# Optimization experiments

Measured on AMD Instinct MI355X. Metric: run time of the kernel, lower is better.

The kernel has to match this reference:

```python
import jax, jax.numpy as jnp
import numpy as np

N = 100000      # nodes
E = 1600000     # edges
IN_DIM = 256
HID = 64
NCLS = 32


def setup_inputs() -> dict:
    key = jax.random.key(0)
    ks = jax.random.split(key, 7)
    features = jax.random.normal(ks[0], (N, IN_DIM), dtype=jnp.float32)
    hidden_prev = jax.random.normal(ks[1], (N, HID), dtype=jnp.float32)
    adj_indices = jax.random.randint(ks[2], (2, E), 0, N, dtype=jnp.int32)
    # torch.rand init, scaled by 0.1 to keep activations numerically sane
    W0 = jax.random.uniform(ks[3], (IN_DIM, HID), dtype=jnp.float32) * 0.1
    W1 = jax.random.uniform(ks[4], (HID, HID), dtype=jnp.float32) * 0.1
    W2 = jax.random.uniform(ks[5], (HID, NCLS), dtype=jnp.float32) * 0.1
    att_w = jax.random.uniform(ks[6], (2 * HID, 1), dtype=jnp.float32) * 0.1
    return {"features": features, "hidden_prev": hidden_prev,
            "adj_indices": adj_indices, "W0": W0, "W1": W1, "W2": W2,
            "att_w": att_w}


def _edge_softmax(scores, rows, n):
    # sparse softmax over dim=1 of an NxN COO: normalize per source row
    m = jax.ops.segment_max(scores, rows, num_segments=n)
    ex = jnp.exp(scores - m[rows])
    s = jax.ops.segment_sum(ex, rows, num_segments=n)
    return ex / s[rows]


def _compute_attention(hfeat, adj_indices, att_w):
    src, dst = adj_indices[0], adj_indices[1]
    h = hfeat.shape[1]
    # cat(f_src, f_dst) @ att_w == f_src @ w_a + f_dst @ w_b ; project per-node
    proj_a = hfeat @ att_w[:h, 0]   # [N]
    proj_b = hfeat @ att_w[h:, 0]   # [N]
    scores = jax.nn.leaky_relu(proj_a[src] + proj_b[dst])  # [E]
    return _edge_softmax(scores, src, hfeat.shape[0])


def _spmm(att_vals, adj_indices, x):
    # out[i] = sum_{(i,j) in E} att * x[j]
    src, dst = adj_indices[0], adj_indices[1]
    return jax.ops.segment_sum(att_vals[:, None] * x[dst], src,
                               num_segments=x.shape[0])


def reference(features, hidden_prev, adj_indices, W0, W1, W2, att_w):
    att = _compute_attention(hidden_prev, adj_indices, att_w)  # [E]
    h = features
    for W in (W0, W1, W2):
        h = jax.nn.elu(_spmm(att, adj_indices, h @ W))
    return jax.nn.log_softmax(h, axis=1)
```

## Files before the change

### kernel.cpp

```cpp
#include <hip/hip_runtime.h>
#include <math.h>

#define HIDN 64
#define NCLS_K 32
#define INDIM 256
#define BSHIFT 7
#define MAXBUCK 1024
#define BUCK_CAP 4096
#define DSTBITS 17
#define DSTMASK ((1 << DSTBITS) - 1)
#define SCB 512

typedef unsigned int uint;
typedef unsigned short ushort;
typedef __attribute__((ext_vector_type(8))) short short8v;
typedef __attribute__((ext_vector_type(4))) float f32x4;

__device__ inline ushort f2bf(float f) {
  uint u = __float_as_uint(f);
  return (ushort)((u + 0x7FFFu + ((u >> 16) & 1u)) >> 16);
}
__device__ inline float bf2f(ushort h) { return __uint_as_float(((uint)h) << 16); }

__global__ __launch_bounds__(256) void proj_kernel(const float* __restrict__ hid,
    const float* __restrict__ attw, float* __restrict__ pa, float* __restrict__ pb, int n) {
  int wid  = (blockIdx.x * blockDim.x + threadIdx.x) >> 6;
  int lane = threadIdx.x & 63;
  if (wid >= n) return;
  float v = hid[(size_t)wid * HIDN + lane];
  float a = v * attw[lane];
  float b = v * attw[HIDN + lane];
  #pragma unroll
  for (int off = 32; off >= 1; off >>= 1) {
    a += __shfl_xor(a, off, 64);
    b += __shfl_xor(b, off, 64);
  }
  if (lane == 0) { pa[wid] = a; pb[wid] = b; }
}

__global__ __launch_bounds__(256) void hist2(const int* __restrict__ src,
    int* __restrict__ hmatT, int e, int nb, int nper) {
  __shared__ int h[MAXBUCK];
  int lo = blockIdx.x * nper;
  int hi = min(e, lo + nper);
  for (int j = threadIdx.x; j < nb; j += 256) h[j] = 0;
  __syncthreads();
  for (int i = lo + threadIdx.x; i < hi; i += 256)
    atomicAdd(&h[src[i] >> BSHIFT], 1);
  __syncthreads();
  for (int j = threadIdx.x; j < nb; j += 256)
    hmatT[(size_t)j * SCB + blockIdx.x] = h[j];
}

__global__ __launch_bounds__(256) void col_scan(int* __restrict__ hmatT,
    int* __restrict__ bcnt, int nb) {
  constexpr int PER = SCB / 64;
  int wv = blockIdx.x * 4 + (threadIdx.x >> 6);
  if (wv >= nb) return;
  int lane = threadIdx.x & 63;
  int* col = hmatT + (size_t)wv * SCB + lane * PER;
  int v[PER];
  int s = 0;
  #pragma unroll
  for (int q = 0; q < PER; ++q) { v[q] = col[q]; s += v[q]; }
  int x = s;
  #pragma unroll
  for (int off = 1; off < 64; off <<= 1) {
    int t = __shfl_up(x, off, 64);
    if (lane >= off) x += t;
  }
  int pre = x - s;
  #pragma unroll
  for (int q = 0; q < PER; ++q) { int t = v[q]; col[q] = pre; pre += t; }
  if (lane == 63) bcnt[wv] = pre;
}

__global__ __launch_bounds__(1024) void scan_buckets(const int* __restrict__ bcnt,
    int* __restrict__ bbase, int* __restrict__ rowp, int nb, int n, int e) {
  __shared__ int sm[1024];
  int tid = threadIdx.x;
  int v = (tid < nb) ? bcnt[tid] : 0;
  sm[tid] = v;
  __syncthreads();
  for (int off = 1; off < 1024; off <<= 1) {
    int t = (tid >= off) ? sm[tid - off] : 0;
    __syncthreads();
    sm[tid] += t;
    __syncthreads();
  }
  if (tid < nb) bbase[tid] = sm[tid] - v;
  if (tid == 0) { bbase[nb] = e; rowp[n] = e; }
}

__global__ __launch_bounds__(256) void scatter2(const int* __restrict__ src,
    const int* __restrict__ dst, const int* __restrict__ hmatT,
    const int* __restrict__ bbase, int* __restrict__ pairs, int e, int nb, int nper) {
  __shared__ int h[MAXBUCK];
  int lo = blockIdx.x * nper;
  int hi = min(e, lo + nper);
  for (int j = threadIdx.x; j < nb; j += 256)
    h[j] = bbase[j] + hmatT[(size_t)j * SCB + blockIdx.x];
  __syncthreads();
  for (int i = lo + threadIdx.x; i < hi; i += 256) {
    int s = src[i];
    int pos = atomicAdd(&h[s >> BSHIFT], 1);
    pairs[pos] = ((s & 127) << DSTBITS) | dst[i];
  }
}

__global__ __launch_bounds__(256) void build_csr(const int* __restrict__ pairs,
    const int* __restrict__ bbase, int* __restrict__ rowp,
    int* __restrict__ dstc, int n) {
  __shared__ int hist[128];
  __shared__ int cur[128];
  __shared__ int ord[BUCK_CAP];
  int b = blockIdx.x;
  int tid = threadIdx.x;
  int base = bbase[b];
  int m = bbase[b + 1] - base;
  if (tid < 128) hist[tid] = 0;
  __syncthreads();
  for (int i = tid; i < m; i += 256)
    atomicAdd(&hist[pairs[base + i] >> DSTBITS], 1);
  __syncthreads();
  int own = (tid < 128) ? hist[tid] : 0;
  for (int off = 1; off < 128; off <<= 1) {
    int t = (tid < 128 && tid >= off) ? hist[tid - off] : 0;
    __syncthreads();
    if (tid < 128) hist[tid] += t;
    __syncthreads();
  }
  if (tid < 128) {
    int excl = hist[tid] - own;
    cur[tid] = excl;
    int s = (b << BSHIFT) + tid;
    if (s < n) rowp[s] = base + excl;
  }
  __syncthreads();
  for (int i = tid; i < m; i += 256) {
    int key = pairs[base + i];
    int pos = atomicAdd(&cur[key >> DSTBITS], 1);
    ord[pos] = key;
  }
  __syncthreads();
  for (int i = tid; i < m; i += 256) dstc[base + i] = ord[i];
}

__device__ inline int wave_sort64(int key, int lane) {
  #pragma unroll
  for (int k = 2; k <= 64; k <<= 1) {
    #pragma unroll
    for (int j = k >> 1; j > 0; j >>= 1) {
      int p = __shfl_xor(key, j, 64);
      bool up    = ((lane & k) == 0);
      bool lower = ((lane & j) == 0);
      int mn = min(key, p), mx = max(key, p);
      key = (lower == up) ? mn : mx;
    }
  }
  return key;
}

__global__ __launch_bounds__(256) void att_softmax(const float* __restrict__ pa,
    const float* __restrict__ pb, int* __restrict__ dstc,
    const int* __restrict__ rowp, ushort* __restrict__ attb, int n) {
  int wid  = (blockIdx.x * blockDim.x + threadIdx.x) >> 6;
  int lane = threadIdx.x & 63;
  if (wid >= n) return;
  int start = rowp[wid], end = rowp[wid + 1];
  int c = end - start;
  if (c <= 0) return;
  float pai = pa[wid];
  if (c <= 64) {
    int e = start + lane;
    int key = (lane < c) ? dstc[e] : 0x7FFFFFFF;
    key = wave_sort64(key, lane);
    float s = -3.0e38f;
    if (lane < c) {
      dstc[e] = key;
      float v = pai + pb[key & DSTMASK];
      s = v > 0.f ? v : 0.01f * v;
    }
    float m = s;
    #pragma unroll
    for (int off = 32; off >= 1; off >>= 1) m = fmaxf(m, __shfl_xor(m, off, 64));
    float ex = (lane < c) ? expf(s - m) : 0.f;
    float sum = ex;
    #pragma unroll
    for (int off = 32; off >= 1; off >>= 1) sum += __shfl_xor(sum, off, 64);
    if (lane < c) attb[e] = f2bf(ex / sum);
    return;
  }
  float m = -3.0e38f;
  for (int base = start; base < end; base += 64) {
    int e = base + lane;
    int key = (e < end) ? dstc[e] : 0x7FFFFFFF;
    key = wave_sort64(key, lane);
    float s = -3.0e38f;
    if (e < end) {
      dstc[e] = key;
      float v = pai + pb[key & DSTMASK];
      s = v > 0.f ? v : 0.01f * v;
      attb[e] = f2bf(s);
    }
    m = fmaxf(m, s);
  }
  #pragma unroll
  for (int off = 32; off >= 1; off >>= 1) m = fmaxf(m, __shfl_xor(m, off, 64));
  float sum = 0.f;
  for (int base = start; base < end; base += 64) {
    int e = base + lane;
    float ex = 0.f;
    if (e < end) { ex = expf(bf2f(attb[e]) - m); attb[e] = f2bf(ex); }
    sum += ex;
  }
  #pragma unroll
  for (int off = 32; off >= 1; off >>= 1) sum += __shfl_xor(sum, off, 64);
  float inv = 1.f / sum;
  for (int base = start; base < end; base += 64) {
    int e = base + lane;
    if (e < end) attb[e] = f2bf(bf2f(attb[e]) * inv);
  }
}

__global__ __launch_bounds__(256) void reorder16(int* __restrict__ dstc,
    ushort* __restrict__ attb, const int* __restrict__ rowp, int n) {
  int g = blockIdx.x * 4 + (threadIdx.x >> 6);
  int row0 = g * 16;
  if (row0 >= n) return;
  int lane = threadIdx.x & 63;
  int nr = min(16, n - row0);
  int start = rowp[row0];
  int end   = rowp[row0 + nr];
  int m = end - start;
  if (m <= 0) return;
  int myd = (lane < nr) ? (rowp[row0 + lane + 1] - rowp[row0 + lane]) : 0;
  int maxd = myd;
  #pragma unroll
  for (int off = 32; off >= 1; off >>= 1) maxd = max(maxd, __shfl_xor(maxd, off, 64));
  if (maxd > 63 || m > 12 * 64) return;
  int cnt = 0;
  #pragma unroll
  for (int rr = 0; rr < 16; ++rr) cnt += (__shfl(myd, rr, 64) > lane) ? 1 : 0;
  int C = cnt;
  #pragma unroll
  for (int off = 1; off < 64; off <<= 1) {
    int t = __shfl_up(C, off, 64);
    if (lane >= off) C += t;
  }
  C -= cnt;
  int key[12]; ushort av[12]; int pos[12]; bool val[12];
  #pragma unroll
  for (int q = 0; q < 12; ++q) {
    int i = start + lane + q * 64;
    val[q] = (i < end);
    int ic = val[q] ? i : start;
    int k = dstc[ic];
    av[q] = attb[ic];
    int r = (k >> DSTBITS) & 15;
    int j = (ic - rowp[row0 + r]) & 63;
    int rank = 0;
    #pragma unroll
    for (int rp = 0; rp < 16; ++rp) {
      int drp = __shfl(myd, rp, 64);
      rank += (rp < r && drp > j) ? 1 : 0;
    }
    int Cj = __shfl(C, j, 64);
    key[q] = k;
    pos[q] = start + Cj + rank;
  }
  asm volatile("s_waitcnt vmcnt(0)" ::: "memory");
  #pragma unroll
  for (int q = 0; q < 12; ++q) {
    if (val[q]) { dstc[pos[q]] = key[q]; attb[pos[q]] = av[q]; }
  }
}

template <int K, int TJ>
__global__ __launch_bounds__(256) void gemm_mfma(const float* __restrict__ A,
    const float* __restrict__ W, ushort* __restrict__ Xb, int n) {
  constexpr int KP = K + 8;
  constexpr int NCB = TJ / 16;
  __shared__ ushort Wt[TJ][KP];
  const int tid = threadIdx.x;
  for (int idx = tid; idx < K * TJ; idx += 256) {
    int k = idx / TJ, j = idx % TJ;
    Wt[j][k] = f2bf(W[idx]);
  }
  __syncthreads();
  const int wv   = blockIdx.x * 4 + (tid >> 6);
  const int row0 = wv * 16;
  if (row0 >= n) return;
  const int lane = tid & 63;
  const int r    = lane & 15;
  const int kg   = lane >> 4;
  const int rowA = min(row0 + r, n - 1);
  const float* ap = A + (size_t)rowA * K + kg * 8;

  f32x4 acc[NCB];
  #pragma unroll
  for (int c = 0; c < NCB; ++c) acc[c] = (f32x4)(0.f);

  #pragma unroll
  for (int ks = 0; ks < K / 32; ++ks) {
    float4 a0 = *reinterpret_cast<const float4*>(ap + ks * 32);
    float4 a1 = *reinterpret_cast<const float4*>(ap + ks * 32 + 4);
    union { short8v v; ushort u[8]; } af;
    af.u[0] = f2bf(a0.x); af.u[1] = f2bf(a0.y);
    af.u[2] = f2bf(a0.z); af.u[3] = f2bf(a0.w);
    af.u[4] = f2bf(a1.x); af.u[5] = f2bf(a1.y);
    af.u[6] = f2bf(a1.z); af.u[7] = f2bf(a1.w);
    #pragma unroll
    for (int c = 0; c < NCB; ++c) {
      short8v bf = *reinterpret_cast<const short8v*>(&Wt[c * 16 + r][ks * 32 + kg * 8]);
      acc[c] = __builtin_amdgcn_mfma_f32_16x16x32_bf16(af.v, bf, acc[c], 0, 0, 0);
    }
  }
  #pragma unroll
  for (int c = 0; c < NCB; ++c) {
    #pragma unroll
    for (int i = 0; i < 4; ++i) {
      int rowS = row0 + kg * 4 + i;
      if (rowS < n) Xb[(size_t)rowS * TJ + c * 16 + r] = f2bf(acc[c][i]);
    }
  }
}

template <int TJ, bool FINAL>
__global__ __launch_bounds__(256) void spmm_mfma(const ushort* __restrict__ Xb,
    const ushort* __restrict__ attb, const int* __restrict__ dstc,
    const int* __restrict__ rowp, float* __restrict__ out, int n) {
  constexpr int NCB = TJ / 16;
  constexpr int CH  = TJ / 8;
  constexpr int EPP = 64 / CH;
  constexpr int RS  = TJ + 4;
  __shared__ ushort Xs[4][32 * RS];
  const int tid   = threadIdx.x;
  const int wslot = tid >> 6;
  const int g     = blockIdx.x * 4 + wslot;
  const int row0  = g * 16;
  if (row0 >= n) return;
  const int lane = tid & 63;
  const int r    = lane & 15;
  const int kg   = lane >> 4;
  const int start = rowp[row0];
  const int end   = rowp[min(row0 + 16, n)];
  ushort* xs = Xs[wslot];
  const int cg = lane % CH;
  const int ce = lane / CH;

  f32x4 acc[NCB];
  #pragma unroll
  for (int c = 0; c < NCB; ++c) acc[c] = (f32x4)(0.f);

  for (int base = start; base < end; base += 32) {
    #pragma unroll
    for (int p = 0; p < CH / 2; ++p) {
      int el  = p * EPP + ce;
      int idx = min(base + el, end - 1);
      int d   = dstc[idx] & DSTMASK;
      uint4 u = *reinterpret_cast<const uint4*>(Xb + (size_t)d * TJ + cg * 8);
      *reinterpret_cast<uint4*>(&xs[el * RS + cg * 8]) = u;
    }
    int sbase = base + 8 * kg;
    union { short8v v; ushort u[8]; } af;
    #pragma unroll
    for (int j = 0; j < 8; ++j) {
      int e = sbase + j;
      bool valid = e < end;
      int idx = valid ? e : (end - 1);
      int v = dstc[idx];
      ushort a = attb[idx];
      int rid = (v >> DSTBITS) & 15;
      af.u[j] = (valid && rid == r) ? a : (ushort)0;
    }
    #pragma unroll
    for (int c = 0; c < NCB; ++c) {
      union { short8v v; ushort u[8]; } bf;
      #pragma unroll
      for (int i = 0; i < 8; ++i)
        bf.u[i] = xs[(8 * kg + i) * RS + c * 16 + r];
      acc[c] = __builtin_amdgcn_mfma_f32_16x16x32_bf16(af.v, bf.v, acc[c], 0, 0, 0);
    }
  }
  #pragma unroll
  for (int c = 0; c < NCB; ++c)
    #pragma unroll
    for (int i = 0; i < 4; ++i)
      acc[c][i] = acc[c][i] > 0.f ? acc[c][i] : (expf(acc[c][i]) - 1.f);
  if (!FINAL) {
    #pragma unroll
    for (int c = 0; c < NCB; ++c)
      #pragma unroll
      for (int i = 0; i < 4; ++i) {
        int rowS = row0 + kg * 4 + i;
        if (rowS < n) out[(size_t)rowS * TJ + c * 16 + r] = acc[c][i];
      }
  } else {
    #pragma unroll
    for (int i = 0; i < 4; ++i) {
      float m = acc[0][i];
      #pragma unroll
      for (int c = 1; c < NCB; ++c) m = fmaxf(m, acc[c][i]);
      #pragma unroll
      for (int off = 1; off < 16; off <<= 1) m = fmaxf(m, __shfl_xor(m, off));
      float s = 0.f;
      #pragma unroll
      for (int c = 0; c < NCB; ++c) s += expf(acc[c][i] - m);
      #pragma unroll
      for (int off = 1; off < 16; off <<= 1) s += __shfl_xor(s, off);
      float lg = m + logf(s);
      int rowS = row0 + kg * 4 + i;
      if (rowS < n) {
        #pragma unroll
        for (int c = 0; c < NCB; ++c)
          out[(size_t)rowS * TJ + c * 16 + r] = acc[c][i] - lg;
      }
    }
  }
}

extern "C" void kernel_launch(void* const* d_in, const int* in_sizes, int n_in,
                              void* d_out, int out_size, void* d_ws, size_t ws_size,
                              hipStream_t stream) {
  const float* features = (const float*)d_in[0];
  const float* hidden   = (const float*)d_in[1];
  const int*   adj      = (const int*)d_in[2];
  const float* W0       = (const float*)d_in[3];
  const float* W1       = (const float*)d_in[4];
  const float* W2       = (const float*)d_in[5];
  const float* attw     = (const float*)d_in[6];
  float* out = (float*)d_out;

  const int N = in_sizes[1] / HIDN;
  const int E = in_sizes[2] / 2;
  const int* src = adj;
  const int* dst = adj + E;
  const int NBUCK = (N + 127) >> BSHIFT;
  const int NB2   = ((NBUCK + 15) / 16) * 16;
  const int nper  = (E + SCB - 1) / SCB;

  int*   rowp  = (int*)d_ws;
  int*   bbase = rowp + (N + 16);
  int*   bcnt  = bbase + (NB2 + 16);
  int*   hmatT = bcnt + NB2;
  int*   dstc  = hmatT + (size_t)NBUCK * SCB;
  ushort* attb = (ushort*)(dstc + E);
  float* Xf    = (float*)(attb) + (E / 2 + 16);
  float* H     = Xf + (size_t)N * HIDN;
  ushort* Xb   = (ushort*)Xf;
  int*   pairs = (int*)Xf;
  float* pa    = H;
  float* pb    = H + N;

  dim3 blk(256);
  const int gridWave = (N + 3) / 4;
  const int gridG16  = ((N + 15) / 16 + 3) / 4;

  proj_kernel<<<gridWave, blk, 0, stream>>>(hidden, attw, pa, pb, N);
  hist2<<<SCB, blk, 0, stream>>>(src, hmatT, E, NBUCK, nper);
  col_scan<<<(NBUCK + 3) / 4, blk, 0, stream>>>(hmatT, bcnt, NBUCK);
  scan_buckets<<<1, 1024, 0, stream>>>(bcnt, bbase, rowp, NBUCK, N, E);
  scatter2<<<SCB, blk, 0, stream>>>(src, dst, hmatT, bbase, pairs, E, NBUCK, nper);
  build_csr<<<NBUCK, blk, 0, stream>>>(pairs, bbase, rowp, dstc, N);
  att_softmax<<<gridWave, blk, 0, stream>>>(pa, pb, dstc, rowp, attb, N);
  reorder16<<<gridG16, blk, 0, stream>>>(dstc, attb, rowp, N);

  gemm_mfma<INDIM, HIDN><<<gridG16, blk, 0, stream>>>(features, W0, Xb, N);
  spmm_mfma<HIDN, false><<<gridG16, blk, 0, stream>>>(Xb, attb, dstc, rowp, H, N);
  gemm_mfma<HIDN, HIDN><<<gridG16, blk, 0, stream>>>(H, W1, Xb, N);
  spmm_mfma<HIDN, false><<<gridG16, blk, 0, stream>>>(Xb, attb, dstc, rowp, H, N);
  gemm_mfma<HIDN, NCLS_K><<<gridG16, blk, 0, stream>>>(H, W2, Xb, N);
  spmm_mfma<NCLS_K, true><<<gridG16, blk, 0, stream>>>(Xb, attb, dstc, rowp, out, N);
}
```

Baseline: 294.1 us.

## Store hidden activations in bf16 and widen SpMM edge chunks with shuffled metadata

The intermediate SpMM outputs are now written as bf16 instead of fp32, and a new GEMM variant reads bf16 activations directly, which halves the traffic of the H round trips. The SpMM loop now handles 64 edges per iteration. Each lane loads one edge's index and attention value once and broadcasts them with wave shuffles, instead of reloading them for every element. All gather loads are issued before the LDS stores so more memory requests are in flight. The cost is extra rounding of the hidden activations to bf16, plus a larger LDS buffer and more registers per wave.

```diff
diff --git a/kernel.cpp b/kernel.cpp
--- a/kernel.cpp
+++ b/kernel.cpp
@@ -326,15 +326,59 @@
   }
 }
 
+template <int K, int TJ>
+__global__ __launch_bounds__(256) void gemm_mfma_bf16(const ushort* __restrict__ A,
+    const float* __restrict__ W, ushort* __restrict__ Xb, int n) {
+  constexpr int KP = K + 8;
+  constexpr int NCB = TJ / 16;
+  __shared__ ushort Wt[TJ][KP];
+  const int tid = threadIdx.x;
+  for (int idx = tid; idx < K * TJ; idx += 256) {
+    int k = idx / TJ, j = idx % TJ;
+    Wt[j][k] = f2bf(W[idx]);
+  }
+  __syncthreads();
+  const int wv   = blockIdx.x * 4 + (tid >> 6);
+  const int row0 = wv * 16;
+  if (row0 >= n) return;
+  const int lane = tid & 63;
+  const int r    = lane & 15;
+  const int kg   = lane >> 4;
+  const int rowA = min(row0 + r, n - 1);
+  const ushort* ap = A + (size_t)rowA * K + kg * 8;
+
+  f32x4 acc[NCB];
+  #pragma unroll
+  for (int c = 0; c < NCB; ++c) acc[c] = (f32x4)(0.f);
+
+  #pragma unroll
+  for (int ks = 0; ks < K / 32; ++ks) {
+    short8v av = *reinterpret_cast<const short8v*>(ap + ks * 32);
+    #pragma unroll
+    for (int c = 0; c < NCB; ++c) {
+      short8v bf = *reinterpret_cast<const short8v*>(&Wt[c * 16 + r][ks * 32 + kg * 8]);
+      acc[c] = __builtin_amdgcn_mfma_f32_16x16x32_bf16(av, bf, acc[c], 0, 0, 0);
+    }
+  }
+  #pragma unroll
+  for (int c = 0; c < NCB; ++c) {
+    #pragma unroll
+    for (int i = 0; i < 4; ++i) {
+      int rowS = row0 + kg * 4 + i;
+      if (rowS < n) Xb[(size_t)rowS * TJ + c * 16 + r] = f2bf(acc[c][i]);
+    }
+  }
+}
+
 template <int TJ, bool FINAL>
 __global__ __launch_bounds__(256) void spmm_mfma(const ushort* __restrict__ Xb,
     const ushort* __restrict__ attb, const int* __restrict__ dstc,
-    const int* __restrict__ rowp, float* __restrict__ out, int n) {
+    const int* __restrict__ rowp, void* __restrict__ outp, int n) {
   constexpr int NCB = TJ / 16;
   constexpr int CH  = TJ / 8;
   constexpr int EPP = 64 / CH;
   constexpr int RS  = TJ + 4;
-  __shared__ ushort Xs[4][32 * RS];
+  __shared__ ushort Xs[4][64 * RS];
   const int tid   = threadIdx.x;
   const int wslot = tid >> 6;
   const int g     = blockIdx.x * 4 + wslot;
@@ -353,34 +397,44 @@
   #pragma unroll
   for (int c = 0; c < NCB; ++c) acc[c] = (f32x4)(0.f);
 
-  for (int base = start; base < end; base += 32) {
-    #pragma unroll
-    for (int p = 0; p < CH / 2; ++p) {
-      int el  = p * EPP + ce;
-      int idx = min(base + el, end - 1);
-      int d   = dstc[idx] & DSTMASK;
-      uint4 u = *reinterpret_cast<const uint4*>(Xb + (size_t)d * TJ + cg * 8);
-      *reinterpret_cast<uint4*>(&xs[el * RS + cg * 8]) = u;
-    }
-    int sbase = base + 8 * kg;
-    union { short8v v; ushort u[8]; } af;
-    #pragma unroll
-    for (int j = 0; j < 8; ++j) {
-      int e = sbase + j;
-      bool valid = e < end;
-      int idx = valid ? e : (end - 1);
-      int v = dstc[idx];
-      ushort a = attb[idx];
-      int rid = (v >> DSTBITS) & 15;
-      af.u[j] = (valid && rid == r) ? a : (ushort)0;
-    }
-    #pragma unroll
-    for (int c = 0; c < NCB; ++c) {
-      union { short8v v; ushort u[8]; } bf;
-      #pragma unroll
-      for (int i = 0; i < 8; ++i)
-        bf.u[i] = xs[(8 * kg + i) * RS + c * 16 + r];
-      acc[c] = __builtin_amdgcn_mfma_f32_16x16x32_bf16(af.v, bf.v, acc[c], 0, 0, 0);
+  for (int base = start; base < end; base += 64) {
+    int idx  = min(base + lane, end - 1);
+    int kful = dstc[idx];
+    int aful = (int)attb[idx];
+    uint4 u[CH];
+    #pragma unroll
+    for (int p = 0; p < CH; ++p) {
+      int el = p * EPP + ce;
+      int d  = __shfl(kful, el, 64) & DSTMASK;
+      u[p] = *reinterpret_cast<const uint4*>(Xb + (size_t)d * TJ + cg * 8);
+    }
+    #pragma unroll
+    for (int p = 0; p < CH; ++p) {
+      int el = p * EPP + ce;
+      *reinterpret_cast<uint4*>(&xs[el * RS + cg * 8]) = u[p];
+    }
+    #pragma unroll
+    for (int h = 0; h < 2; ++h) {
+      int sb = h * 32 + 8 * kg;
+      if (base + h * 32 < end) {
+        union { short8v v; ushort u[8]; } af;
+        #pragma unroll
+        for (int j = 0; j < 8; ++j) {
+          int kk = __shfl(kful, sb + j, 64);
+          int aa = __shfl(aful, sb + j, 64);
+          bool valid = (base + sb + j) < end;
+          int rid = (kk >> DSTBITS) & 15;
+          af.u[j] = (valid && rid == r) ? (ushort)aa : (ushort)0;
+        }
+        #pragma unroll
+        for (int c = 0; c < NCB; ++c) {
+          union { short8v v; ushort u[8]; } bf;
+          #pragma unroll
+          for (int i = 0; i < 8; ++i)
+            bf.u[i] = xs[(sb + i) * RS + c * 16 + r];
+          acc[c] = __builtin_amdgcn_mfma_f32_16x16x32_bf16(af.v, bf.v, acc[c], 0, 0, 0);
+        }
+      }
     }
   }
   #pragma unroll
@@ -389,14 +443,16 @@
     for (int i = 0; i < 4; ++i)
       acc[c][i] = acc[c][i] > 0.f ? acc[c][i] : (expf(acc[c][i]) - 1.f);
   if (!FINAL) {
+    ushort* out = (ushort*)outp;
     #pragma unroll
     for (int c = 0; c < NCB; ++c)
       #pragma unroll
       for (int i = 0; i < 4; ++i) {
         int rowS = row0 + kg * 4 + i;
-        if (rowS < n) out[(size_t)rowS * TJ + c * 16 + r] = acc[c][i];
+        if (rowS < n) out[(size_t)rowS * TJ + c * 16 + r] = f2bf(acc[c][i]);
       }
   } else {
+    float* out = (float*)outp;
     #pragma unroll
     for (int i = 0; i < 4; ++i) {
       float m = acc[0][i];
@@ -447,11 +503,12 @@
   int*   dstc  = hmatT + (size_t)NBUCK * SCB;
   ushort* attb = (ushort*)(dstc + E);
   float* Xf    = (float*)(attb) + (E / 2 + 16);
-  float* H     = Xf + (size_t)N * HIDN;
+  float* Hf    = Xf + (size_t)N * HIDN;
   ushort* Xb   = (ushort*)Xf;
+  ushort* Hb   = (ushort*)Hf;
   int*   pairs = (int*)Xf;
-  float* pa    = H;
-  float* pb    = H + N;
+  float* pa    = Hf;
+  float* pb    = Hf + N;
 
   dim3 blk(256);
   const int gridWave = (N + 3) / 4;
@@ -467,9 +524,9 @@
   reorder16<<<gridG16, blk, 0, stream>>>(dstc, attb, rowp, N);
 
   gemm_mfma<INDIM, HIDN><<<gridG16, blk, 0, stream>>>(features, W0, Xb, N);
-  spmm_mfma<HIDN, false><<<gridG16, blk, 0, stream>>>(Xb, attb, dstc, rowp, H, N);
-  gemm_mfma<HIDN, HIDN><<<gridG16, blk, 0, stream>>>(H, W1, Xb, N);
-  spmm_mfma<HIDN, false><<<gridG16, blk, 0, stream>>>(Xb, attb, dstc, rowp, H, N);
-  gemm_mfma<HIDN, NCLS_K><<<gridG16, blk, 0, stream>>>(H, W2, Xb, N);
+  spmm_mfma<HIDN, false><<<gridG16, blk, 0, stream>>>(Xb, attb, dstc, rowp, Hb, N);
+  gemm_mfma_bf16<HIDN, HIDN><<<gridG16, blk, 0, stream>>>(Hb, W1, Xb, N);
+  spmm_mfma<HIDN, false><<<gridG16, blk, 0, stream>>>(Xb, attb, dstc, rowp, Hb, N);
+  gemm_mfma_bf16<HIDN, NCLS_K><<<gridG16, blk, 0, stream>>>(Hb, W2, Xb, N);
   spmm_mfma<NCLS_K, true><<<gridG16, blk, 0, stream>>>(Xb, attb, dstc, rowp, out, N);
 }
```

New measurement: 295.5 us. Within noise of the previous version (+0.5%).
